# Optimization experiments

Hardware: AMD Instinct MI355X
Metric: run time of the kernel (lower is better)

Reference implementation:

```python
import jax, jax.numpy as jnp
import numpy as np

D_M, D_K, D_V, HEADS = 1024, 64, 64, 16
B, S = 2, 2048


def setup_inputs() -> dict:
    key = jax.random.key(0)
    ks = jax.random.split(key, 5)
    x = jax.random.normal(ks[0], (B, S, D_M), dtype=jnp.float32)
    # per-head projection weights (original deep-copies one rand init per head;
    # we give each head independent weights, matching the per-head param structure)
    Wk = jax.random.uniform(ks[1], (HEADS, D_M, D_K), dtype=jnp.float32)
    Wq = jax.random.uniform(ks[2], (HEADS, D_M, D_K), dtype=jnp.float32)
    Wv = jax.random.uniform(ks[3], (HEADS, D_M, D_V), dtype=jnp.float32)
    Wo = jax.random.uniform(ks[4], (HEADS * D_V, D_M), dtype=jnp.float32)
    return {"x": x, "Wk": Wk, "Wq": Wq, "Wv": Wv, "Wo": Wo}


def reference(x, Wk, Wq, Wv, Wo):
    # per-head QKV projections, batched over heads: [B,H,S,d]
    q = jnp.einsum("bsm,hmk->bhsk", x, Wq)
    k = jnp.einsum("bsm,hmk->bhsk", x, Wk)
    v = jnp.einsum("bsm,hmv->bhsv", x, Wv)
    scale = 1.0 / jnp.sqrt(jnp.asarray(q.shape[-1], dtype=q.dtype))
    scores = jnp.einsum("bhsk,bhtk->bhst", q, k) * scale  # [B,H,S,S]
    attn = jax.nn.softmax(scores, axis=-1)
    ctx = jnp.einsum("bhst,bhtv->bhsv", attn, v)  # [B,H,S,d_v]
    # concat heads -> [B,S,H*d_v], then output projection
    ctx = jnp.transpose(ctx, (0, 2, 1, 3)).reshape(x.shape[0], x.shape[1], -1)
    return jnp.einsum("bsc,cm->bsm", ctx, Wo)
```

## Files before the change

kernel.cpp:

```cpp
#include <hip/hip_runtime.h>
#include <hip/hip_bf16.h>
#include <stdint.h>

#define DM   1024
#define DKV  64
#define HEADS 16
#define BATCH 2
#define SEQ  2048
#define BS   (BATCH*SEQ)
#define BHD  (BATCH*HEADS)

typedef __attribute__((ext_vector_type(8))) short bf16x8;
typedef __attribute__((ext_vector_type(4))) short bf16x4;
typedef __attribute__((ext_vector_type(4))) float f32x4;

__device__ inline unsigned fb(float f) { union { float f; unsigned u; } v; v.f = f; return v.u; }

__device__ inline unsigned short bf16_rtn(float f) {
  unsigned u = fb(f);
  unsigned r = u + 0x7fffu + ((u >> 16) & 1u);
  return (unsigned short)(r >> 16);
}
__device__ inline float bf16_to_f(unsigned short h) {
  union { unsigned u; float f; } v; v.u = ((unsigned)h) << 16; return v.f;
}
__device__ inline void split_bf16(float x, unsigned short& hi, unsigned short& lo) {
  hi = bf16_rtn(x);
  lo = bf16_rtn(x - bf16_to_f(hi));
}
__device__ inline unsigned pack2_bf16(float lo_elem, float hi_elem) {
  return __builtin_amdgcn_perm(fb(hi_elem) + 0x8000u, fb(lo_elem) + 0x8000u, 0x07060302u);
}

__device__ inline float fast_exp2(float x) {
#if __has_builtin(__builtin_amdgcn_exp2f)
  return __builtin_amdgcn_exp2f(x);
#else
  return exp2f(x);
#endif
}

__device__ inline f32x4 mfma16x16x16_bf16(bf16x4 a, bf16x4 b, f32x4 c) {
#if __has_builtin(__builtin_amdgcn_mfma_f32_16x16x16bf16_1k)
  return __builtin_amdgcn_mfma_f32_16x16x16bf16_1k(a, b, c, 0, 0, 0);
#else
  asm volatile("v_mfma_f32_16x16x16_bf16 %0, %1, %2, %0" : "+v"(c) : "v"(a), "v"(b));
  return c;
#endif
}

__device__ inline void stage16(const unsigned short* g, unsigned short* lds_base, int lane) {
#if __has_builtin(__builtin_amdgcn_global_load_lds)
  __builtin_amdgcn_global_load_lds((__attribute__((address_space(1))) void*)(g),
                                   (__attribute__((address_space(3))) void*)(lds_base),
                                   16, 0, 0);
#else
  *(bf16x8*)(lds_base + lane * 8) = *(const bf16x8*)g;
#endif
}

__device__ inline int swz(int row, int chunk) {
  return row * 64 + (((chunk ^ (row & 7)) & 7) << 3);
}

__global__ void cvt_x_split(const float* __restrict__ x,
                            unsigned short* __restrict__ xh, unsigned short* __restrict__ xl) {
  int i = (blockIdx.x * 256 + threadIdx.x) * 8;
  bf16x8 oh, ol;
  #pragma unroll
  for (int j = 0; j < 8; ++j) {
    unsigned short hi, lo;
    split_bf16(x[i + j], hi, lo);
    oh[j] = (short)hi; ol[j] = (short)lo;
  }
  *(bf16x8*)(xh + i) = oh;
  *(bf16x8*)(xl + i) = ol;
}

__global__ void pack_qkv_split(const float* __restrict__ Wq, const float* __restrict__ Wk,
                               const float* __restrict__ Wv,
                               unsigned short* __restrict__ Wh, unsigned short* __restrict__ Wl) {
  __shared__ float tile[64][65];
  int bid = blockIdx.x;
  int p = bid >> 8, h = (bid >> 4) & 15, mt = bid & 15;
  const float* W = (p == 0) ? Wq : (p == 1) ? Wk : Wv;
  const float* src = W + (size_t)h * (DM * DKV);
  int t = threadIdx.x;
  int m0 = mt * 64;
  #pragma unroll
  for (int pass = 0; pass < 16; ++pass) {
    int row = pass * 4 + (t >> 6), col = t & 63;
    tile[row][col] = src[(size_t)(m0 + row) * DKV + col];
  }
  __syncthreads();
  int cbase = p * 1024 + h * 64;
  #pragma unroll
  for (int pass = 0; pass < 16; ++pass) {
    int krow = pass * 4 + (t >> 6), mcol = t & 63;
    unsigned short hi, lo;
    split_bf16(tile[mcol][krow], hi, lo);
    size_t idx = (size_t)(cbase + krow) * DM + m0 + mcol;
    Wh[idx] = hi; Wl[idx] = lo;
  }
}

__global__ void pack_wo(const float* __restrict__ Wo, unsigned short* __restrict__ WoT) {
  __shared__ float tile[64][65];
  int ib = blockIdx.x >> 4, jb = blockIdx.x & 15;
  int t = threadIdx.x;
  #pragma unroll
  for (int pass = 0; pass < 16; ++pass) {
    int row = pass * 4 + (t >> 6), col = t & 63;
    tile[row][col] = Wo[(size_t)(ib * 64 + row) * DM + jb * 64 + col];
  }
  __syncthreads();
  #pragma unroll
  for (int pass = 0; pass < 16; ++pass) {
    int a = pass * 4 + (t >> 6), b = t & 63;
    WoT[(size_t)(jb * 64 + a) * DM + ib * 64 + b] = bf16_rtn(tile[b][a]);
  }
}

__global__ __launch_bounds__(256, 2)
void gemm_qk(const unsigned short* __restrict__ Ah, const unsigned short* __restrict__ Al,
             const unsigned short* __restrict__ Bh, const unsigned short* __restrict__ Bl,
             unsigned short* __restrict__ Qh, unsigned short* __restrict__ Ql,
             unsigned short* __restrict__ Kh, unsigned short* __restrict__ Kl) {
  __shared__ unsigned short AsH[128 * 64], AsL[128 * 64];
  __shared__ unsigned short BsH[128 * 64], BsL[128 * 64];
  const int tid = threadIdx.x;
  const int w = tid >> 6, lane = tid & 63;
  const int quad = lane >> 4, l16 = lane & 15;
  const int wm = w >> 1, wn = w & 1;
  const int bn = blockIdx.x, bm = blockIdx.y;

  f32x4 acc[4][4];
  #pragma unroll
  for (int i = 0; i < 4; ++i)
    #pragma unroll
    for (int j = 0; j < 4; ++j) acc[i][j] = (f32x4){0.f, 0.f, 0.f, 0.f};

  const int r8 = lane >> 3, c8 = lane & 7;
  const int cs = c8 ^ r8;
  const size_t offA = (size_t)(bm * 128 + w * 32 + r8) * DM + cs * 8;
  const size_t offB = (size_t)(bn * 128 + w * 32 + r8) * DM + cs * 8;

  for (int kk = 0; kk < DM / 64; ++kk) {
    #pragma unroll
    for (int ps = 0; ps < 4; ++ps) {
      unsigned short* dA = AsH + (w * 32 + ps * 8) * 64;
      unsigned short* dAl = AsL + (w * 32 + ps * 8) * 64;
      unsigned short* dB = BsH + (w * 32 + ps * 8) * 64;
      unsigned short* dBl = BsL + (w * 32 + ps * 8) * 64;
      stage16(Ah + offA + kk * 64 + ps * 8 * DM, dA,  lane);
      stage16(Al + offA + kk * 64 + ps * 8 * DM, dAl, lane);
      stage16(Bh + offB + kk * 64 + ps * 8 * DM, dB,  lane);
      stage16(Bl + offB + kk * 64 + ps * 8 * DM, dBl, lane);
    }
    asm volatile("s_waitcnt vmcnt(0)" ::: "memory");
    __syncthreads();
    #pragma unroll
    for (int ks = 0; ks < 2; ++ks) {
      bf16x8 afh[4], afl[4], bfh[4], bfl[4];
      #pragma unroll
      for (int mt = 0; mt < 4; ++mt) {
        int row = wm * 64 + mt * 16 + l16;
        int ad = row * 64 + ((((ks * 4 + quad) ^ (row & 7)) & 7) << 3);
        afh[mt] = *(const bf16x8*)(AsH + ad);
        afl[mt] = *(const bf16x8*)(AsL + ad);
      }
      #pragma unroll
      for (int nt = 0; nt < 4; ++nt) {
        int row = wn * 64 + nt * 16 + l16;
        int ad = row * 64 + ((((ks * 4 + quad) ^ (row & 7)) & 7) << 3);
        bfh[nt] = *(const bf16x8*)(BsH + ad);
        bfl[nt] = *(const bf16x8*)(BsL + ad);
      }
      #pragma unroll
      for (int mt = 0; mt < 4; ++mt)
        #pragma unroll
        for (int nt = 0; nt < 4; ++nt) {
          acc[mt][nt] = __builtin_amdgcn_mfma_f32_16x16x32_bf16(afh[mt], bfh[nt], acc[mt][nt], 0, 0, 0);
          acc[mt][nt] = __builtin_amdgcn_mfma_f32_16x16x32_bf16(afh[mt], bfl[nt], acc[mt][nt], 0, 0, 0);
          acc[mt][nt] = __builtin_amdgcn_mfma_f32_16x16x32_bf16(afl[mt], bfh[nt], acc[mt][nt], 0, 0, 0);
        }
    }
    __syncthreads();
  }

  const float SCL = 0.18033688011112042f;
  #pragma unroll
  for (int mt = 0; mt < 4; ++mt) {
    int m_g = bm * 128 + wm * 64 + mt * 16 + quad * 4;
    #pragma unroll
    for (int nt = 0; nt < 4; ++nt) {
      int n_g = bn * 128 + wn * 64 + nt * 16 + l16;
      int p = n_g >> 10, h = (n_g >> 6) & 15, k = n_g & 63;
      #pragma unroll
      for (int r = 0; r < 4; ++r) {
        int row = m_g + r;
        int b = row >> 11, s = row & 2047;
        int bh = b * HEADS + h;
        float v = acc[mt][nt][r];
        size_t idx = ((size_t)(bh * SEQ + s)) * DKV + k;
        unsigned short hi, lo;
        if (p == 0) {
          split_bf16(v * SCL, hi, lo);
          Qh[idx] = hi; Ql[idx] = lo;
        } else {
          split_bf16(v, hi, lo);
          Kh[idx] = hi; Kl[idx] = lo;
        }
      }
    }
  }
}

__global__ __launch_bounds__(256, 2)
void gemm_v(const unsigned short* __restrict__ A, const unsigned short* __restrict__ Bt,
            unsigned short* __restrict__ Vt) {
  __shared__ unsigned short As[64 * 64];
  __shared__ unsigned short Bs[128 * 64];
  const int tid = threadIdx.x;
  const int w = tid >> 6, lane = tid & 63;
  const int quad = lane >> 4, l16 = lane & 15;
  const int wm = w >> 1, wn = w & 1;
  const int bn = blockIdx.x, bm = blockIdx.y;

  f32x4 acc[2][4];
  #pragma unroll
  for (int i = 0; i < 2; ++i)
    #pragma unroll
    for (int j = 0; j < 4; ++j) acc[i][j] = (f32x4){0.f, 0.f, 0.f, 0.f};

  const int r8 = lane >> 3, c8 = lane & 7;
  const int cs = c8 ^ r8;
  const size_t offA = (size_t)(bm * 64 + w * 16 + r8) * DM + cs * 8;
  const size_t offB = (size_t)(bn * 128 + w * 32 + r8) * DM + cs * 8;

  for (int kk = 0; kk < DM / 64; ++kk) {
    #pragma unroll
    for (int ps = 0; ps < 2; ++ps)
      stage16(A + offA + kk * 64 + ps * 8 * DM, As + (w * 16 + ps * 8) * 64, lane);
    #pragma unroll
    for (int ps = 0; ps < 4; ++ps)
      stage16(Bt + offB + kk * 64 + ps * 8 * DM, Bs + (w * 32 + ps * 8) * 64, lane);
    asm volatile("s_waitcnt vmcnt(0)" ::: "memory");
    __syncthreads();
    #pragma unroll
    for (int ks = 0; ks < 2; ++ks) {
      bf16x8 af[2], bfr[4];
      #pragma unroll
      for (int mt = 0; mt < 2; ++mt) {
        int row = wm * 32 + mt * 16 + l16;
        af[mt] = *(const bf16x8*)(As + row * 64 + ((((ks * 4 + quad) ^ (row & 7)) & 7) << 3));
      }
      #pragma unroll
      for (int nt = 0; nt < 4; ++nt) {
        int row = wn * 64 + nt * 16 + l16;
        bfr[nt] = *(const bf16x8*)(Bs + row * 64 + ((((ks * 4 + quad) ^ (row & 7)) & 7) << 3));
      }
      #pragma unroll
      for (int mt = 0; mt < 2; ++mt)
        #pragma unroll
        for (int nt = 0; nt < 4; ++nt)
          acc[mt][nt] = __builtin_amdgcn_mfma_f32_16x16x32_bf16(af[mt], bfr[nt], acc[mt][nt], 0, 0, 0);
    }
    __syncthreads();
  }

  #pragma unroll
  for (int mt = 0; mt < 2; ++mt) {
    int m_g = bm * 64 + wm * 32 + mt * 16 + quad * 4;
    #pragma unroll
    for (int nt = 0; nt < 4; ++nt) {
      int n_g = bn * 128 + wn * 64 + nt * 16 + l16;
      int h = n_g >> 6, k = n_g & 63;
      #pragma unroll
      for (int r = 0; r < 4; ++r) {
        int row = m_g + r;
        int b = row >> 11, s = row & 2047;
        int bh = b * HEADS + h;
        Vt[((size_t)(bh * DKV + k)) * SEQ + s] = bf16_rtn(acc[mt][nt][r]);
      }
    }
  }
}

__global__ __launch_bounds__(256, 2)
void flash(const unsigned short* __restrict__ Qh, const unsigned short* __restrict__ Ql,
           const unsigned short* __restrict__ Kh, const unsigned short* __restrict__ Kl,
           const unsigned short* __restrict__ Vt, unsigned short* __restrict__ ctx) {
  __shared__ unsigned short KtH[2][64 * 64], KtL[2][64 * 64], Vts[2][64 * 64];
  const int tid = threadIdx.x;
  const int w = tid >> 6, lane = tid & 63, quad = lane >> 4, l16 = lane & 15;
  const int bh = blockIdx.x;
  const int q0 = blockIdx.y * 128;

  bf16x8 qfh[2][2], qfl[2][2];
  #pragma unroll
  for (int qt = 0; qt < 2; ++qt) {
    int qrow = q0 + w * 32 + qt * 16 + l16;
    size_t base = ((size_t)(bh * SEQ + qrow)) * DKV + quad * 8;
    qfh[qt][0] = *(const bf16x8*)(Qh + base);
    qfh[qt][1] = *(const bf16x8*)(Qh + base + 32);
    qfl[qt][0] = *(const bf16x8*)(Ql + base);
    qfl[qt][1] = *(const bf16x8*)(Ql + base + 32);
  }

  float m_run[2] = {-1e30f, -1e30f};
  float l_run[2] = {0.f, 0.f};
  f32x4 acc[2][4];
  #pragma unroll
  for (int qt = 0; qt < 2; ++qt)
    #pragma unroll
    for (int vt = 0; vt < 4; ++vt) acc[qt][vt] = (f32x4){0.f, 0.f, 0.f, 0.f};

  const int srow = w * 16 + (lane >> 3);
  const int csrc = (lane & 7) ^ (lane >> 3);
  const unsigned short* kh_src = Kh + ((size_t)(bh * SEQ) + srow) * DKV + csrc * 8;
  const unsigned short* kl_src = Kl + ((size_t)(bh * SEQ) + srow) * DKV + csrc * 8;
  const unsigned short* v_src  = Vt + ((size_t)(bh * DKV) + srow) * SEQ + csrc * 8;

  #define STAGE(buf, kt0)                                                     \
    do {                                                                      \
      unsigned short* dH = &KtH[buf][(w * 16) * 64];                          \
      unsigned short* dL = &KtL[buf][(w * 16) * 64];                          \
      unsigned short* dV = &Vts[buf][(w * 16) * 64];                          \
      stage16(kh_src + (size_t)(kt0) * DKV,            dH,       lane);       \
      stage16(kh_src + (size_t)(kt0) * DKV + 8 * DKV,  dH + 512, lane);       \
      stage16(kl_src + (size_t)(kt0) * DKV,            dL,       lane);       \
      stage16(kl_src + (size_t)(kt0) * DKV + 8 * DKV,  dL + 512, lane);       \
      stage16(v_src  + (kt0),                          dV,       lane);       \
      stage16(v_src  + (kt0) + 8 * SEQ,                dV + 512, lane);       \
    } while (0)

  STAGE(0, 0);
  asm volatile("s_waitcnt vmcnt(0)" ::: "memory");
  __syncthreads();
  int cur = 0;

  for (int kt = 0; kt < SEQ / 64; ++kt) {
    if (kt + 1 < SEQ / 64) STAGE(cur ^ 1, (kt + 1) * 64);

    const unsigned short* kH = KtH[cur];
    const unsigned short* kL = KtL[cur];
    const unsigned short* vS = Vts[cur];

    f32x4 st[4][2];
    __builtin_amdgcn_s_setprio(1);
    #pragma unroll
    for (int mt = 0; mt < 4; ++mt) {
      int rowA = mt * 16 + l16;
      bf16x8 kah0 = *(const bf16x8*)(kH + swz(rowA, quad));
      bf16x8 kah1 = *(const bf16x8*)(kH + swz(rowA, quad + 4));
      bf16x8 kal0 = *(const bf16x8*)(kL + swz(rowA, quad));
      bf16x8 kal1 = *(const bf16x8*)(kL + swz(rowA, quad + 4));
      #pragma unroll
      for (int qt = 0; qt < 2; ++qt) {
        f32x4 c = (f32x4){0.f, 0.f, 0.f, 0.f};
        c = __builtin_amdgcn_mfma_f32_16x16x32_bf16(kah0, qfh[qt][0], c, 0, 0, 0);
        c = __builtin_amdgcn_mfma_f32_16x16x32_bf16(kah1, qfh[qt][1], c, 0, 0, 0);
        c = __builtin_amdgcn_mfma_f32_16x16x32_bf16(kah0, qfl[qt][0], c, 0, 0, 0);
        c = __builtin_amdgcn_mfma_f32_16x16x32_bf16(kah1, qfl[qt][1], c, 0, 0, 0);
        c = __builtin_amdgcn_mfma_f32_16x16x32_bf16(kal0, qfh[qt][0], c, 0, 0, 0);
        c = __builtin_amdgcn_mfma_f32_16x16x32_bf16(kal1, qfh[qt][1], c, 0, 0, 0);
        st[mt][qt] = c;
      }
    }
    __builtin_amdgcn_s_setprio(0);

    bf16x4 pb[2][4];
    #pragma unroll
    for (int qt = 0; qt < 2; ++qt) {
      float cm = -1e30f;
      #pragma unroll
      for (int mt = 0; mt < 4; ++mt)
        #pragma unroll
        for (int r = 0; r < 4; ++r) cm = fmaxf(cm, st[mt][qt][r]);
      cm = fmaxf(cm, __shfl_xor(cm, 16));
      cm = fmaxf(cm, __shfl_xor(cm, 32));
      bool upd = cm > m_run[qt];
      float mn = upd ? cm : m_run[qt];
      float ssum = 0.f;
      #pragma unroll
      for (int mt = 0; mt < 4; ++mt) {
        float p0 = fast_exp2(st[mt][qt][0] - mn);
        float p1 = fast_exp2(st[mt][qt][1] - mn);
        float p2 = fast_exp2(st[mt][qt][2] - mn);
        float p3 = fast_exp2(st[mt][qt][3] - mn);
        ssum += (p0 + p1) + (p2 + p3);
        union { bf16x4 v; unsigned u2[2]; } pk;
        pk.u2[0] = pack2_bf16(p0, p1);
        pk.u2[1] = pack2_bf16(p2, p3);
        pb[qt][mt] = pk.v;
      }
      ssum += __shfl_xor(ssum, 16);
      ssum += __shfl_xor(ssum, 32);
      if (__ballot(upd)) {
        float alpha = fast_exp2(m_run[qt] - mn);
        m_run[qt] = mn;
        l_run[qt] = l_run[qt] * alpha + ssum;
        #pragma unroll
        for (int vt = 0; vt < 4; ++vt) acc[qt][vt] = acc[qt][vt] * alpha;
      } else {
        l_run[qt] += ssum;
      }
    }

    __builtin_amdgcn_s_setprio(1);
    #pragma unroll
    for (int vt = 0; vt < 4; ++vt) {
      #pragma unroll
      for (int mt = 0; mt < 4; ++mt) {
        int row = vt * 16 + l16;
        int addr = row * 64 + ((((mt * 2 + (quad >> 1)) ^ (row & 7)) & 7) << 3) + (quad & 1) * 4;
        bf16x4 va = *(const bf16x4*)(vS + addr);
        #pragma unroll
        for (int qt = 0; qt < 2; ++qt)
          acc[qt][vt] = mfma16x16x16_bf16(va, pb[qt][mt], acc[qt][vt]);
      }
    }
    __builtin_amdgcn_s_setprio(0);

    asm volatile("s_waitcnt vmcnt(0)" ::: "memory");
    __syncthreads();
    cur ^= 1;
  }
  #undef STAGE

  int h = bh & 15, b = bh >> 4;
  #pragma unroll
  for (int qt = 0; qt < 2; ++qt) {
    float inv = 1.0f / l_run[qt];
    int bs = b * SEQ + q0 + w * 32 + qt * 16 + l16;
    #pragma unroll
    for (int vt = 0; vt < 4; ++vt) {
      union { bf16x4 v; unsigned u2[2]; } pk;
      pk.u2[0] = pack2_bf16(acc[qt][vt][0] * inv, acc[qt][vt][1] * inv);
      pk.u2[1] = pack2_bf16(acc[qt][vt][2] * inv, acc[qt][vt][3] * inv);
      *(bf16x4*)(ctx + (size_t)bs * DM + h * 64 + vt * 16 + quad * 4) = pk.v;
    }
  }
}

__global__ __launch_bounds__(256, 2)
void gemm_out(const unsigned short* __restrict__ A, const unsigned short* __restrict__ Bt,
              float* __restrict__ out) {
  __shared__ unsigned short As[64 * 64];
  __shared__ unsigned short Bs[128 * 64];
  const int tid = threadIdx.x;
  const int w = tid >> 6, lane = tid & 63;
  const int quad = lane >> 4, l16 = lane & 15;
  const int wm = w >> 1, wn = w & 1;
  const int bn = blockIdx.x, bm = blockIdx.y;

  f32x4 acc[2][4];
  #pragma unroll
  for (int i = 0; i < 2; ++i)
    #pragma unroll
    for (int j = 0; j < 4; ++j) acc[i][j] = (f32x4){0.f, 0.f, 0.f, 0.f};

  const int r8 = lane >> 3, c8 = lane & 7;
  const int cs = c8 ^ r8;
  const size_t offA = (size_t)(bm * 64 + w * 16 + r8) * DM + cs * 8;
  const size_t offB = (size_t)(bn * 128 + w * 32 + r8) * DM + cs * 8;

  for (int kk = 0; kk < DM / 64; ++kk) {
    #pragma unroll
    for (int ps = 0; ps < 2; ++ps)
      stage16(A + offA + kk * 64 + ps * 8 * DM, As + (w * 16 + ps * 8) * 64, lane);
    #pragma unroll
    for (int ps = 0; ps < 4; ++ps)
      stage16(Bt + offB + kk * 64 + ps * 8 * DM, Bs + (w * 32 + ps * 8) * 64, lane);
    asm volatile("s_waitcnt vmcnt(0)" ::: "memory");
    __syncthreads();
    #pragma unroll
    for (int ks = 0; ks < 2; ++ks) {
      bf16x8 af[2], bfr[4];
      #pragma unroll
      for (int mt = 0; mt < 2; ++mt) {
        int row = wm * 32 + mt * 16 + l16;
        af[mt] = *(const bf16x8*)(As + row * 64 + ((((ks * 4 + quad) ^ (row & 7)) & 7) << 3));
      }
      #pragma unroll
      for (int nt = 0; nt < 4; ++nt) {
        int row = wn * 64 + nt * 16 + l16;
        bfr[nt] = *(const bf16x8*)(Bs + row * 64 + ((((ks * 4 + quad) ^ (row & 7)) & 7) << 3));
      }
      #pragma unroll
      for (int mt = 0; mt < 2; ++mt)
        #pragma unroll
        for (int nt = 0; nt < 4; ++nt)
          acc[mt][nt] = __builtin_amdgcn_mfma_f32_16x16x32_bf16(af[mt], bfr[nt], acc[mt][nt], 0, 0, 0);
    }
    __syncthreads();
  }

  #pragma unroll
  for (int mt = 0; mt < 2; ++mt) {
    int m_g = bm * 64 + wm * 32 + mt * 16 + quad * 4;
    #pragma unroll
    for (int nt = 0; nt < 4; ++nt) {
      int n_g = bn * 128 + wn * 64 + nt * 16 + l16;
      #pragma unroll
      for (int r = 0; r < 4; ++r)
        out[(size_t)(m_g + r) * DM + n_g] = acc[mt][nt][r];
    }
  }
}

extern "C" void kernel_launch(void* const* d_in, const int* in_sizes, int n_in,
                              void* d_out, int out_size, void* d_ws, size_t ws_size,
                              hipStream_t stream) {
  const float* x  = (const float*)d_in[0];
  const float* Wk = (const float*)d_in[1];
  const float* Wq = (const float*)d_in[2];
  const float* Wv = (const float*)d_in[3];
  const float* Wo = (const float*)d_in[4];
  float* out = (float*)d_out;

  unsigned short* xh  = (unsigned short*)d_ws;
  unsigned short* xl  = xh  + (size_t)BS * DM;
  unsigned short* Wh  = xl  + (size_t)BS * DM;
  unsigned short* Wl  = Wh  + (size_t)3 * DM * DM;
  unsigned short* WoT = Wl  + (size_t)3 * DM * DM;
  unsigned short* Qh  = WoT + (size_t)DM * DM;
  unsigned short* Ql  = Qh  + (size_t)BHD * SEQ * DKV;
  unsigned short* Kh  = Ql  + (size_t)BHD * SEQ * DKV;
  unsigned short* Kl  = Kh  + (size_t)BHD * SEQ * DKV;
  unsigned short* Vtb = Kl  + (size_t)BHD * SEQ * DKV;
  unsigned short* ctx = Vtb + (size_t)BHD * SEQ * DKV;

  cvt_x_split<<<(BS * DM) / (256 * 8), 256, 0, stream>>>(x, xh, xl);
  pack_qkv_split<<<3 * 16 * 16, 256, 0, stream>>>(Wq, Wk, Wv, Wh, Wl);
  pack_wo<<<16 * 16, 256, 0, stream>>>(Wo, WoT);
  gemm_qk<<<dim3(16, 32), 256, 0, stream>>>(xh, xl, Wh, Wl, Qh, Ql, Kh, Kl);
  gemm_v<<<dim3(8, 64), 256, 0, stream>>>(xh, Wh + (size_t)2048 * DM, Vtb);
  flash<<<dim3(BHD, SEQ / 128), 256, 0, stream>>>(Qh, Ql, Kh, Kl, Vtb, ctx);
  gemm_out<<<dim3(8, 64), 256, 0, stream>>>(ctx, WoT, out);
}
```

Baseline: 242.0 us.

## Split key range across two warp groups in flash kernel and merge in LDS

The flash kernel now runs 512 threads per block, with two groups of four waves each processing half of the key sequence for the same query tile. Partial softmax states are merged through shared memory at the end. V is single-buffered and loaded after a barrier, while K stays double-buffered. The aim is more parallelism per query tile. In exchange it uses more LDS per block, adds an extra barrier per iteration, and V loads no longer overlap compute.

```diff
diff --git a/kernel.cpp b/kernel.cpp
--- a/kernel.cpp
+++ b/kernel.cpp
@@ -287,20 +287,24 @@
   }
 }
 
-__global__ __launch_bounds__(256, 2)
+__global__ __launch_bounds__(512, 4)
 void flash(const unsigned short* __restrict__ Qh, const unsigned short* __restrict__ Ql,
            const unsigned short* __restrict__ Kh, const unsigned short* __restrict__ Kl,
            const unsigned short* __restrict__ Vt, unsigned short* __restrict__ ctx) {
-  __shared__ unsigned short KtH[2][64 * 64], KtL[2][64 * 64], Vts[2][64 * 64];
+  __shared__ __attribute__((aligned(16))) unsigned char smem[81920];
   const int tid = threadIdx.x;
   const int w = tid >> 6, lane = tid & 63, quad = lane >> 4, l16 = lane & 15;
+  const int g = w >> 2, wq = w & 3;
   const int bh = blockIdx.x;
   const int q0 = blockIdx.y * 128;
+  const int k0 = g * 1024;
+
+  unsigned char* gb = smem + g * 40960;
 
   bf16x8 qfh[2][2], qfl[2][2];
   #pragma unroll
   for (int qt = 0; qt < 2; ++qt) {
-    int qrow = q0 + w * 32 + qt * 16 + l16;
+    int qrow = q0 + wq * 32 + qt * 16 + l16;
     size_t base = ((size_t)(bh * SEQ + qrow)) * DKV + quad * 8;
     qfh[qt][0] = *(const bf16x8*)(Qh + base);
     qfh[qt][1] = *(const bf16x8*)(Qh + base + 32);
@@ -316,36 +320,41 @@
     #pragma unroll
     for (int vt = 0; vt < 4; ++vt) acc[qt][vt] = (f32x4){0.f, 0.f, 0.f, 0.f};
 
-  const int srow = w * 16 + (lane >> 3);
+  const int srow = wq * 16 + (lane >> 3);
   const int csrc = (lane & 7) ^ (lane >> 3);
-  const unsigned short* kh_src = Kh + ((size_t)(bh * SEQ) + srow) * DKV + csrc * 8;
-  const unsigned short* kl_src = Kl + ((size_t)(bh * SEQ) + srow) * DKV + csrc * 8;
-  const unsigned short* v_src  = Vt + ((size_t)(bh * DKV) + srow) * SEQ + csrc * 8;
-
-  #define STAGE(buf, kt0)                                                     \
-    do {                                                                      \
-      unsigned short* dH = &KtH[buf][(w * 16) * 64];                          \
-      unsigned short* dL = &KtL[buf][(w * 16) * 64];                          \
-      unsigned short* dV = &Vts[buf][(w * 16) * 64];                          \
-      stage16(kh_src + (size_t)(kt0) * DKV,            dH,       lane);       \
-      stage16(kh_src + (size_t)(kt0) * DKV + 8 * DKV,  dH + 512, lane);       \
-      stage16(kl_src + (size_t)(kt0) * DKV,            dL,       lane);       \
-      stage16(kl_src + (size_t)(kt0) * DKV + 8 * DKV,  dL + 512, lane);       \
-      stage16(v_src  + (kt0),                          dV,       lane);       \
-      stage16(v_src  + (kt0) + 8 * SEQ,                dV + 512, lane);       \
+  const unsigned short* kh_src = Kh + ((size_t)(bh * SEQ) + k0 + srow) * DKV + csrc * 8;
+  const unsigned short* kl_src = Kl + ((size_t)(bh * SEQ) + k0 + srow) * DKV + csrc * 8;
+  const unsigned short* v_src  = Vt + ((size_t)(bh * DKV) + srow) * SEQ + k0 + csrc * 8;
+
+  #define STAGE_K(buf, it0)                                                    \
+    do {                                                                       \
+      unsigned short* dH = (unsigned short*)(gb + (buf) * 8192) + wq * 1024;   \
+      unsigned short* dL = (unsigned short*)(gb + 16384 + (buf) * 8192) + wq * 1024; \
+      stage16(kh_src + (size_t)(it0) * 64 * DKV,            dH,       lane);   \
+      stage16(kh_src + (size_t)(it0) * 64 * DKV + 8 * DKV,  dH + 512, lane);   \
+      stage16(kl_src + (size_t)(it0) * 64 * DKV,            dL,       lane);   \
+      stage16(kl_src + (size_t)(it0) * 64 * DKV + 8 * DKV,  dL + 512, lane);   \
     } while (0)
-
-  STAGE(0, 0);
+  #define STAGE_V(it0)                                                         \
+    do {                                                                       \
+      unsigned short* dV = (unsigned short*)(gb + 32768) + wq * 1024;          \
+      stage16(v_src + (it0) * 64,            dV,       lane);                  \
+      stage16(v_src + (it0) * 64 + 8 * SEQ,  dV + 512, lane);                  \
+    } while (0)
+
+  STAGE_K(0, 0);
+  STAGE_V(0);
   asm volatile("s_waitcnt vmcnt(0)" ::: "memory");
   __syncthreads();
   int cur = 0;
 
-  for (int kt = 0; kt < SEQ / 64; ++kt) {
-    if (kt + 1 < SEQ / 64) STAGE(cur ^ 1, (kt + 1) * 64);
-
-    const unsigned short* kH = KtH[cur];
-    const unsigned short* kL = KtL[cur];
-    const unsigned short* vS = Vts[cur];
+  const unsigned short* vS = (const unsigned short*)(gb + 32768);
+
+  for (int it = 0; it < 16; ++it) {
+    if (it + 1 < 16) STAGE_K(cur ^ 1, it + 1);
+
+    const unsigned short* kH = (const unsigned short*)(gb + cur * 8192);
+    const unsigned short* kL = (const unsigned short*)(gb + 16384 + cur * 8192);
 
     f32x4 st[4][2];
     __builtin_amdgcn_s_setprio(1);
@@ -423,23 +432,55 @@
     }
     __builtin_amdgcn_s_setprio(0);
 
-    asm volatile("s_waitcnt vmcnt(0)" ::: "memory");
+    __syncthreads();
+    if (it + 1 < 16) {
+      STAGE_V(it + 1);
+      asm volatile("s_waitcnt vmcnt(0)" ::: "memory");
+    }
     __syncthreads();
     cur ^= 1;
   }
-  #undef STAGE
-
-  int h = bh & 15, b = bh >> 4;
-  #pragma unroll
-  for (int qt = 0; qt < 2; ++qt) {
-    float inv = 1.0f / l_run[qt];
-    int bs = b * SEQ + q0 + w * 32 + qt * 16 + l16;
-    #pragma unroll
-    for (int vt = 0; vt < 4; ++vt) {
-      union { bf16x4 v; unsigned u2[2]; } pk;
-      pk.u2[0] = pack2_bf16(acc[qt][vt][0] * inv, acc[qt][vt][1] * inv);
-      pk.u2[1] = pack2_bf16(acc[qt][vt][2] * inv, acc[qt][vt][3] * inv);
-      *(bf16x4*)(ctx + (size_t)bs * DM + h * 64 + vt * 16 + quad * 4) = pk.v;
+  #undef STAGE_K
+  #undef STAGE_V
+
+  float* sAcc = (float*)smem;
+  float* sML  = (float*)(smem + 32768);
+  if (g == 1) {
+    #pragma unroll
+    for (int qt = 0; qt < 2; ++qt) {
+      #pragma unroll
+      for (int vt = 0; vt < 4; ++vt)
+        *(f32x4*)(sAcc + ((wq * 2 + qt) * 4 + vt) * 256 + l16 * 16 + quad * 4) = acc[qt][vt];
+      if (quad == 0) {
+        sML[(wq * 2 + qt) * 32 + l16 * 2]     = m_run[qt];
+        sML[(wq * 2 + qt) * 32 + l16 * 2 + 1] = l_run[qt];
+      }
+    }
+  }
+  __syncthreads();
+  if (g == 0) {
+    int h = bh & 15, b = bh >> 4;
+    #pragma unroll
+    for (int qt = 0; qt < 2; ++qt) {
+      float m2 = sML[(wq * 2 + qt) * 32 + l16 * 2];
+      float l2 = sML[(wq * 2 + qt) * 32 + l16 * 2 + 1];
+      float mN = fmaxf(m_run[qt], m2);
+      float a1 = fast_exp2(m_run[qt] - mN);
+      float a2 = fast_exp2(m2 - mN);
+      float inv = 1.0f / (a1 * l_run[qt] + a2 * l2);
+      int bs = b * SEQ + q0 + wq * 32 + qt * 16 + l16;
+      #pragma unroll
+      for (int vt = 0; vt < 4; ++vt) {
+        f32x4 o2 = *(const f32x4*)(sAcc + ((wq * 2 + qt) * 4 + vt) * 256 + l16 * 16 + quad * 4);
+        union { bf16x4 v; unsigned u2[2]; } pk;
+        float e0 = (a1 * acc[qt][vt][0] + a2 * o2[0]) * inv;
+        float e1 = (a1 * acc[qt][vt][1] + a2 * o2[1]) * inv;
+        float e2 = (a1 * acc[qt][vt][2] + a2 * o2[2]) * inv;
+        float e3 = (a1 * acc[qt][vt][3] + a2 * o2[3]) * inv;
+        pk.u2[0] = pack2_bf16(e0, e1);
+        pk.u2[1] = pack2_bf16(e2, e3);
+        *(bf16x4*)(ctx + (size_t)bs * DM + h * 64 + vt * 16 + quad * 4) = pk.v;
+      }
     }
   }
 }
@@ -537,6 +578,6 @@
   pack_wo<<<16 * 16, 256, 0, stream>>>(Wo, WoT);
   gemm_qk<<<dim3(16, 32), 256, 0, stream>>>(xh, xl, Wh, Wl, Qh, Ql, Kh, Kl);
   gemm_v<<<dim3(8, 64), 256, 0, stream>>>(xh, Wh + (size_t)2048 * DM, Vtb);
-  flash<<<dim3(BHD, SEQ / 128), 256, 0, stream>>>(Qh, Ql, Kh, Kl, Vtb, ctx);
+  flash<<<dim3(BHD, SEQ / 128), 512, 0, stream>>>(Qh, Ql, Kh, Kl, Vtb, ctx);
   gemm_out<<<dim3(8, 64), 256, 0, stream>>>(ctx, WoT, out);
 }
```

Measured after the change: 250.6 us. 1.04x slower.

## Software-pipeline attention loop: overlap next tile QK^T with current softmax

Applied to the files above, without the earlier changes.

Restructures the flash-attention inner loop so the QK^T MFMAs for tile t+1 are interleaved with the softmax of tile t. K is staged two tiles ahead and V one tile ahead, with separate buffer indices. The softmax rescale branch (ballot on max update) is made unconditional, and the setprio hints are dropped. The aim is to hide exp/shuffle latency behind matrix-core work, at the cost of extra live registers for a second score tile.

```diff
diff --git a/kernel.cpp b/kernel.cpp
--- a/kernel.cpp
+++ b/kernel.cpp
@@ -322,112 +322,136 @@
   const unsigned short* kl_src = Kl + ((size_t)(bh * SEQ) + srow) * DKV + csrc * 8;
   const unsigned short* v_src  = Vt + ((size_t)(bh * DKV) + srow) * SEQ + csrc * 8;
 
-  #define STAGE(buf, kt0)                                                     \
-    do {                                                                      \
-      unsigned short* dH = &KtH[buf][(w * 16) * 64];                          \
-      unsigned short* dL = &KtL[buf][(w * 16) * 64];                          \
-      unsigned short* dV = &Vts[buf][(w * 16) * 64];                          \
-      stage16(kh_src + (size_t)(kt0) * DKV,            dH,       lane);       \
-      stage16(kh_src + (size_t)(kt0) * DKV + 8 * DKV,  dH + 512, lane);       \
-      stage16(kl_src + (size_t)(kt0) * DKV,            dL,       lane);       \
-      stage16(kl_src + (size_t)(kt0) * DKV + 8 * DKV,  dL + 512, lane);       \
-      stage16(v_src  + (kt0),                          dV,       lane);       \
-      stage16(v_src  + (kt0) + 8 * SEQ,                dV + 512, lane);       \
+  #define STAGE_K(buf, kt0)                                                     \
+    do {                                                                        \
+      unsigned short* dH = &KtH[buf][(w * 16) * 64];                            \
+      unsigned short* dL = &KtL[buf][(w * 16) * 64];                            \
+      stage16(kh_src + (size_t)(kt0) * 64 * DKV,           dH,       lane);     \
+      stage16(kh_src + (size_t)(kt0) * 64 * DKV + 8 * DKV, dH + 512, lane);     \
+      stage16(kl_src + (size_t)(kt0) * 64 * DKV,           dL,       lane);     \
+      stage16(kl_src + (size_t)(kt0) * 64 * DKV + 8 * DKV, dL + 512, lane);     \
     } while (0)
-
-  STAGE(0, 0);
+  #define STAGE_V(buf, kt0)                                                     \
+    do {                                                                        \
+      unsigned short* dV = &Vts[buf][(w * 16) * 64];                            \
+      stage16(v_src + (kt0) * 64,           dV,       lane);                    \
+      stage16(v_src + (kt0) * 64 + 8 * SEQ, dV + 512, lane);                    \
+    } while (0)
+
+  #define QK_HALF(STV, KHP, KLP, MT0)                                           \
+    _Pragma("unroll")                                                           \
+    for (int mt = (MT0); mt < (MT0) + 2; ++mt) {                                \
+      int rowA = mt * 16 + l16;                                                 \
+      bf16x8 kah0 = *(const bf16x8*)((KHP) + swz(rowA, quad));                  \
+      bf16x8 kah1 = *(const bf16x8*)((KHP) + swz(rowA, quad + 4));              \
+      bf16x8 kal0 = *(const bf16x8*)((KLP) + swz(rowA, quad));                  \
+      bf16x8 kal1 = *(const bf16x8*)((KLP) + swz(rowA, quad + 4));              \
+      _Pragma("unroll")                                                         \
+      for (int qt = 0; qt < 2; ++qt) {                                          \
+        f32x4 c = (f32x4){0.f, 0.f, 0.f, 0.f};                                  \
+        c = __builtin_amdgcn_mfma_f32_16x16x32_bf16(kah0, qfh[qt][0], c, 0, 0, 0); \
+        c = __builtin_amdgcn_mfma_f32_16x16x32_bf16(kah1, qfh[qt][1], c, 0, 0, 0); \
+        c = __builtin_amdgcn_mfma_f32_16x16x32_bf16(kah0, qfl[qt][0], c, 0, 0, 0); \
+        c = __builtin_amdgcn_mfma_f32_16x16x32_bf16(kah1, qfl[qt][1], c, 0, 0, 0); \
+        c = __builtin_amdgcn_mfma_f32_16x16x32_bf16(kal0, qfh[qt][0], c, 0, 0, 0); \
+        c = __builtin_amdgcn_mfma_f32_16x16x32_bf16(kal1, qfh[qt][1], c, 0, 0, 0); \
+        (STV)[mt][qt] = c;                                                      \
+      }                                                                         \
+    }
+
+  #define SM_QT(QT)                                                             \
+    {                                                                           \
+      float cm = -1e30f;                                                        \
+      _Pragma("unroll")                                                         \
+      for (int mt = 0; mt < 4; ++mt)                                            \
+        _Pragma("unroll")                                                       \
+        for (int r = 0; r < 4; ++r) cm = fmaxf(cm, st[mt][QT][r]);              \
+      cm = fmaxf(cm, __shfl_xor(cm, 16));                                       \
+      cm = fmaxf(cm, __shfl_xor(cm, 32));                                       \
+      float mn = fmaxf(cm, m_run[QT]);                                          \
+      float ssum = 0.f;                                                         \
+      _Pragma("unroll")                                                         \
+      for (int mt = 0; mt < 4; ++mt) {                                          \
+        float p0 = fast_exp2(st[mt][QT][0] - mn);                               \
+        float p1 = fast_exp2(st[mt][QT][1] - mn);                               \
+        float p2 = fast_exp2(st[mt][QT][2] - mn);                               \
+        float p3 = fast_exp2(st[mt][QT][3] - mn);                               \
+        ssum += (p0 + p1) + (p2 + p3);                                          \
+        union { bf16x4 v; unsigned u2[2]; } pk;                                 \
+        pk.u2[0] = pack2_bf16(p0, p1);                                          \
+        pk.u2[1] = pack2_bf16(p2, p3);                                          \
+        pb[QT][mt] = pk.v;                                                      \
+      }                                                                         \
+      ssum += __shfl_xor(ssum, 16);                                             \
+      ssum += __shfl_xor(ssum, 32);                                             \
+      float alpha = fast_exp2(m_run[QT] - mn);                                  \
+      m_run[QT] = mn;                                                           \
+      l_run[QT] = l_run[QT] * alpha + ssum;                                     \
+      _Pragma("unroll")                                                         \
+      for (int vt = 0; vt < 4; ++vt) acc[QT][vt] = acc[QT][vt] * alpha;         \
+    }
+
+  #define PV_ALL(VSP)                                                           \
+    _Pragma("unroll")                                                           \
+    for (int vt = 0; vt < 4; ++vt)                                              \
+      _Pragma("unroll")                                                         \
+      for (int mt = 0; mt < 4; ++mt) {                                          \
+        int row = vt * 16 + l16;                                                \
+        int addr = row * 64 + ((((mt * 2 + (quad >> 1)) ^ (row & 7)) & 7) << 3) + (quad & 1) * 4; \
+        bf16x4 va = *(const bf16x4*)((VSP) + addr);                             \
+        _Pragma("unroll")                                                       \
+        for (int qt = 0; qt < 2; ++qt)                                          \
+          acc[qt][vt] = mfma16x16x16_bf16(va, pb[qt][mt], acc[qt][vt]);         \
+      }
+
+  STAGE_K(0, 0);
+  STAGE_V(0, 0);
+  STAGE_K(1, 1);
   asm volatile("s_waitcnt vmcnt(0)" ::: "memory");
   __syncthreads();
-  int cur = 0;
-
-  for (int kt = 0; kt < SEQ / 64; ++kt) {
-    if (kt + 1 < SEQ / 64) STAGE(cur ^ 1, (kt + 1) * 64);
-
-    const unsigned short* kH = KtH[cur];
-    const unsigned short* kL = KtL[cur];
-    const unsigned short* vS = Vts[cur];
-
-    f32x4 st[4][2];
-    __builtin_amdgcn_s_setprio(1);
-    #pragma unroll
-    for (int mt = 0; mt < 4; ++mt) {
-      int rowA = mt * 16 + l16;
-      bf16x8 kah0 = *(const bf16x8*)(kH + swz(rowA, quad));
-      bf16x8 kah1 = *(const bf16x8*)(kH + swz(rowA, quad + 4));
-      bf16x8 kal0 = *(const bf16x8*)(kL + swz(rowA, quad));
-      bf16x8 kal1 = *(const bf16x8*)(kL + swz(rowA, quad + 4));
-      #pragma unroll
-      for (int qt = 0; qt < 2; ++qt) {
-        f32x4 c = (f32x4){0.f, 0.f, 0.f, 0.f};
-        c = __builtin_amdgcn_mfma_f32_16x16x32_bf16(kah0, qfh[qt][0], c, 0, 0, 0);
-        c = __builtin_amdgcn_mfma_f32_16x16x32_bf16(kah1, qfh[qt][1], c, 0, 0, 0);
-        c = __builtin_amdgcn_mfma_f32_16x16x32_bf16(kah0, qfl[qt][0], c, 0, 0, 0);
-        c = __builtin_amdgcn_mfma_f32_16x16x32_bf16(kah1, qfl[qt][1], c, 0, 0, 0);
-        c = __builtin_amdgcn_mfma_f32_16x16x32_bf16(kal0, qfh[qt][0], c, 0, 0, 0);
-        c = __builtin_amdgcn_mfma_f32_16x16x32_bf16(kal1, qfh[qt][1], c, 0, 0, 0);
-        st[mt][qt] = c;
-      }
-    }
-    __builtin_amdgcn_s_setprio(0);
+
+  f32x4 st[4][2];
+  QK_HALF(st, KtH[0], KtL[0], 0);
+  QK_HALF(st, KtH[0], KtL[0], 2);
+
+  #pragma unroll 2
+  for (int t = 0; t < SEQ / 64 - 1; ++t) {
+    const int cb = t & 1, nb = (t + 1) & 1;
+    if (t + 2 < SEQ / 64) STAGE_K(cb, t + 2);
+    STAGE_V(nb, t + 1);
+
+    const unsigned short* kHn = KtH[nb];
+    const unsigned short* kLn = KtL[nb];
+    const unsigned short* vS  = Vts[cb];
 
     bf16x4 pb[2][4];
-    #pragma unroll
-    for (int qt = 0; qt < 2; ++qt) {
-      float cm = -1e30f;
-      #pragma unroll
-      for (int mt = 0; mt < 4; ++mt)
-        #pragma unroll
-        for (int r = 0; r < 4; ++r) cm = fmaxf(cm, st[mt][qt][r]);
-      cm = fmaxf(cm, __shfl_xor(cm, 16));
-      cm = fmaxf(cm, __shfl_xor(cm, 32));
-      bool upd = cm > m_run[qt];
-      float mn = upd ? cm : m_run[qt];
-      float ssum = 0.f;
-      #pragma unroll
-      for (int mt = 0; mt < 4; ++mt) {
-        float p0 = fast_exp2(st[mt][qt][0] - mn);
-        float p1 = fast_exp2(st[mt][qt][1] - mn);
-        float p2 = fast_exp2(st[mt][qt][2] - mn);
-        float p3 = fast_exp2(st[mt][qt][3] - mn);
-        ssum += (p0 + p1) + (p2 + p3);
-        union { bf16x4 v; unsigned u2[2]; } pk;
-        pk.u2[0] = pack2_bf16(p0, p1);
-        pk.u2[1] = pack2_bf16(p2, p3);
-        pb[qt][mt] = pk.v;
-      }
-      ssum += __shfl_xor(ssum, 16);
-      ssum += __shfl_xor(ssum, 32);
-      if (__ballot(upd)) {
-        float alpha = fast_exp2(m_run[qt] - mn);
-        m_run[qt] = mn;
-        l_run[qt] = l_run[qt] * alpha + ssum;
-        #pragma unroll
-        for (int vt = 0; vt < 4; ++vt) acc[qt][vt] = acc[qt][vt] * alpha;
-      } else {
-        l_run[qt] += ssum;
-      }
-    }
-
-    __builtin_amdgcn_s_setprio(1);
-    #pragma unroll
-    for (int vt = 0; vt < 4; ++vt) {
-      #pragma unroll
-      for (int mt = 0; mt < 4; ++mt) {
-        int row = vt * 16 + l16;
-        int addr = row * 64 + ((((mt * 2 + (quad >> 1)) ^ (row & 7)) & 7) << 3) + (quad & 1) * 4;
-        bf16x4 va = *(const bf16x4*)(vS + addr);
-        #pragma unroll
-        for (int qt = 0; qt < 2; ++qt)
-          acc[qt][vt] = mfma16x16x16_bf16(va, pb[qt][mt], acc[qt][vt]);
-      }
-    }
-    __builtin_amdgcn_s_setprio(0);
+    f32x4 stn[4][2];
+    SM_QT(0);
+    QK_HALF(stn, kHn, kLn, 0);
+    SM_QT(1);
+    QK_HALF(stn, kHn, kLn, 2);
+    PV_ALL(vS);
+
+    #pragma unroll
+    for (int mt = 0; mt < 4; ++mt)
+      #pragma unroll
+      for (int qt = 0; qt < 2; ++qt) st[mt][qt] = stn[mt][qt];
 
     asm volatile("s_waitcnt vmcnt(0)" ::: "memory");
     __syncthreads();
-    cur ^= 1;
-  }
-  #undef STAGE
+  }
+
+  {
+    bf16x4 pb[2][4];
+    SM_QT(0);
+    SM_QT(1);
+    PV_ALL(Vts[(SEQ / 64 - 1) & 1]);
+  }
+  #undef STAGE_K
+  #undef STAGE_V
+  #undef QK_HALF
+  #undef SM_QT
+  #undef PV_ALL
 
   int h = bh & 15, b = bh >> 4;
   #pragma unroll
```

After: 251.7 us. 4.0% more time.
